# Optimization experiments

Hardware: AMD Instinct MI355X
Metric: run time of the kernel (lower is better)

## Reference

```python
import jax, jax.numpy as jnp
import numpy as np

T, D, L, H, N = 4096, 512, 10, 512, 40960  # tokens, feat dim, max span width, hidden, n_spans
LAMBDA = 0.4


def setup_inputs() -> dict:
    key = jax.random.key(0)
    ks = jax.random.split(key, 12)
    lin = lambda k, i, o: jax.random.normal(k, (i, o), jnp.float32) * 0.02
    return {
        "states": jax.random.normal(ks[0], (T, D), jnp.float32),
        "embeds": jax.random.normal(ks[1], (T, D), jnp.float32),
        "span_starts": jax.random.randint(ks[2], (N,), 0, T - L, jnp.int32),
        "span_widths": jax.random.randint(ks[3], (N,), 0, L, jnp.int32),
        "W_a1": lin(ks[4], D, H), "b_a1": jnp.zeros((H,), jnp.float32),
        "W_a2": lin(ks[5], H, H), "b_a2": jnp.zeros((H,), jnp.float32),
        "w_a3": lin(ks[6], H, 1), "b_a3": jnp.zeros((1,), jnp.float32),
        "W_s1": lin(ks[7], 3 * D, H), "b_s1": jnp.zeros((H,), jnp.float32),
        "W_s2": lin(ks[8], H, H), "b_s2": jnp.zeros((H,), jnp.float32),
        "w_s3": lin(ks[9], H, 1), "b_s3": jnp.zeros((1,), jnp.float32),
    }


def reference(states, embeds, span_starts, span_widths,
              W_a1, b_a1, W_a2, b_a2, w_a3, b_a3,
              W_s1, b_s1, W_s2, b_s2, w_s3, b_s3):
    # SpanAttention MLP: per-token attention logits [T]
    h = jax.nn.relu(states @ W_a1 + b_a1)
    h = jax.nn.relu(h @ W_a2 + b_a2)
    attns = (h @ w_a3 + b_a3)[:, 0]  # [T]

    # Ragged spans vectorized as fixed-width gather + mask.
    offs = jnp.arange(L, dtype=jnp.int32)            # [L]
    idx = span_starts[:, None] + offs[None, :]       # [N, L] token indices (in-range by construction)
    mask = offs[None, :] <= span_widths[:, None]     # [N, L]

    # Per-span masked softmax over attention logits (F.softmax(span_attn, dim=0)).
    logits = jnp.where(mask, attns[idx], -jnp.inf)
    w = jax.nn.softmax(logits, axis=1)               # [N, L]

    # Attention-weighted sum of word EMBEDDINGS over the span.
    attended = jnp.einsum('nl,nld->nd', w, embeds[idx])  # [N, D]

    ends = span_starts + span_widths                 # inclusive end index
    g = jnp.concatenate([states[span_starts], states[ends], attended], axis=-1)  # [N, 3D]

    # Mention score MLP
    s = jax.nn.relu(g @ W_s1 + b_s1)
    s = jax.nn.relu(s @ W_s2 + b_s2)
    scores = (s @ w_s3 + b_s3)[:, 0]                 # [N]

    # prune: keep top LAMBDA*T spans by score, sorted by index (Lee et al. 2017)
    k = int(LAMBDA * T)
    _, top_idx = jax.lax.top_k(scores, k)
    pruned_idx = jnp.sort(top_idx)
    return scores[pruned_idx], g, pruned_idx
```

## Files before the change

kernel.cpp:

```cpp
#include <hip/hip_runtime.h>
#include <hip/hip_bf16.h>
#include <stdint.h>

#define T_TOK 4096
#define D_DIM 512
#define L_SPAN 10
#define H_DIM 512
#define N_SPAN 40960
#define K_TOP 1638
#define CAND_CAP 6144
#define MARGIN 0.01f

typedef __attribute__((ext_vector_type(8))) short bf16x8;
typedef __attribute__((ext_vector_type(4))) float f32x4;

__device__ __forceinline__ ushort f2bf(float x) {
  uint32_t u = __float_as_uint(x);
  return (ushort)((u + 0x7FFFu + ((u >> 16) & 1u)) >> 16);
}
__device__ __forceinline__ float bf2f(ushort s) {
  return __uint_as_float(((uint32_t)s) << 16);
}

template <bool RELU, bool INDEXED>
__global__ __launch_bounds__(256) void sgemm32(
    const float* __restrict__ A, const float* __restrict__ B,
    const float* __restrict__ bias, float* __restrict__ C,
    int Kk, int lda, int ldb, int ldc,
    const uint32_t* __restrict__ rowCnt, const int* __restrict__ rowIdx) {
  const int BM = 32, BN = 64, BK = 32;
  __shared__ float As[BK][BM + 2];
  __shared__ float Bs[BK][BN + 4];

  int tid = threadIdx.x;
  int bn = blockIdx.x, bm = blockIdx.y;

  int cc = INDEXED ? 0 : 0x7fffffff;
  if (rowCnt) {
    cc = (int)*rowCnt;
    if (cc > CAND_CAP) cc = CAND_CAP;
    if (bm * BM >= ((cc + 31) & ~31)) return;
  }

  int tx = tid & 15, ty = tid >> 4;
  int a_m = tid >> 3;
  int a_k2 = tid & 7;
  int b_c4 = tid & 15;
  int b_kr = tid >> 4;

  int slot = bm * BM + a_m;
  const float* aRow;
  if (INDEXED) {
    int grow = (slot < cc) ? rowIdx[slot] : 0;
    aRow = A + (size_t)grow * lda;
  } else {
    aRow = A + (size_t)slot * lda;
  }
  const float* bPtr = B + (size_t)b_kr * ldb + bn * BN + b_c4 * 4;

  float acc[2][4];
#pragma unroll
  for (int i = 0; i < 2; ++i)
#pragma unroll
    for (int j = 0; j < 4; ++j) acc[i][j] = 0.f;

  for (int k0 = 0; k0 < Kk; k0 += BK) {
#pragma unroll
    for (int p = 0; p < 2; ++p) {
      float2 v = *(const float2*)(aRow + k0 + p * 16 + a_k2 * 2);
      As[p * 16 + a_k2 * 2 + 0][a_m] = v.x;
      As[p * 16 + a_k2 * 2 + 1][a_m] = v.y;
    }
#pragma unroll
    for (int p = 0; p < 2; ++p) {
      float4 v = *(const float4*)(bPtr + (size_t)(k0 + p * 16) * ldb);
      *(float4*)&Bs[b_kr + p * 16][b_c4 * 4] = v;
    }
    __syncthreads();

#pragma unroll
    for (int kk = 0; kk < BK; ++kk) {
      float2 a = *(const float2*)&As[kk][ty * 2];
      float4 b = *(const float4*)&Bs[kk][tx * 4];
      acc[0][0] = fmaf(a.x, b.x, acc[0][0]);
      acc[0][1] = fmaf(a.x, b.y, acc[0][1]);
      acc[0][2] = fmaf(a.x, b.z, acc[0][2]);
      acc[0][3] = fmaf(a.x, b.w, acc[0][3]);
      acc[1][0] = fmaf(a.y, b.x, acc[1][0]);
      acc[1][1] = fmaf(a.y, b.y, acc[1][1]);
      acc[1][2] = fmaf(a.y, b.z, acc[1][2]);
      acc[1][3] = fmaf(a.y, b.w, acc[1][3]);
    }
    __syncthreads();
  }

  int col0 = bn * BN + tx * 4;
  float4 bb = *(const float4*)(bias + col0);
#pragma unroll
  for (int i = 0; i < 2; ++i) {
    int row = bm * BM + ty * 2 + i;
    float o0 = acc[i][0] + bb.x;
    float o1 = acc[i][1] + bb.y;
    float o2 = acc[i][2] + bb.z;
    float o3 = acc[i][3] + bb.w;
    if (RELU) {
      o0 = fmaxf(o0, 0.f); o1 = fmaxf(o1, 0.f);
      o2 = fmaxf(o2, 0.f); o3 = fmaxf(o3, 0.f);
    }
    *(float4*)(C + (size_t)row * ldc + col0) = make_float4(o0, o1, o2, o3);
  }
}

__global__ __launch_bounds__(256) void mfma_gemm(
    const ushort* __restrict__ Ab, const ushort* __restrict__ Bb,
    const float* __restrict__ bias, ushort* __restrict__ Out,
    int K, int lda) {
  __shared__ ushort As[128][48];
  __shared__ ushort Bs[64][48];

  int wgl = blockIdx.x;
  int xcd = wgl & 7;
  int s = wgl >> 3;
  int p = ((s >> 3) << 3) | xcd;
  int bn = s & 7;
  int tid = threadIdx.x;
  int w = tid >> 6, l = tid & 63;
  int waveM = w & 1, waveN = w >> 1;
  int lr = l & 15, lg = l >> 4;
  int rowbase = p * 128;

  f32x4 acc[4][2];
#pragma unroll
  for (int m = 0; m < 4; ++m)
#pragma unroll
    for (int n = 0; n < 2; ++n)
#pragma unroll
      for (int r = 0; r < 4; ++r) acc[m][n][r] = 0.f;

  for (int k0 = 0; k0 < K; k0 += 32) {
#pragma unroll
    for (int it = 0; it < 2; ++it) {
      int idx = tid + it * 256;
      int ar = idx >> 2;
      int kc = (idx & 3) * 8;
      const ushort* src = Ab + (size_t)(rowbase + ar) * lda + k0 + kc;
      *(uint4*)&As[ar][kc] = *(const uint4*)src;
    }
    {
      int n = tid & 63;
      int kk0 = (tid >> 6) * 8;
#pragma unroll
      for (int i = 0; i < 8; ++i)
        Bs[n][kk0 + i] = Bb[(size_t)(k0 + kk0 + i) * 512 + bn * 64 + n];
    }
    __syncthreads();

    bf16x8 af[4], bv[2];
#pragma unroll
    for (int m = 0; m < 4; ++m)
      af[m] = *(const bf16x8*)&As[waveM * 64 + m * 16 + lr][lg * 8];
#pragma unroll
    for (int n = 0; n < 2; ++n)
      bv[n] = *(const bf16x8*)&Bs[waveN * 32 + n * 16 + lr][lg * 8];
#pragma unroll
    for (int m = 0; m < 4; ++m)
#pragma unroll
      for (int n = 0; n < 2; ++n)
        acc[m][n] = __builtin_amdgcn_mfma_f32_16x16x32_bf16(af[m], bv[n], acc[m][n], 0, 0, 0);
    __syncthreads();
  }

#pragma unroll
  for (int m = 0; m < 4; ++m) {
    int rg = rowbase + waveM * 64 + m * 16 + lg * 4;
#pragma unroll
    for (int n = 0; n < 2; ++n) {
      int cg = bn * 64 + waveN * 32 + n * 16 + lr;
      float bb = bias[cg];
#pragma unroll
      for (int r = 0; r < 4; ++r) {
        float v = fmaxf(acc[m][n][r] + bb, 0.f);
        Out[(size_t)(rg + r) * 512 + cg] = f2bf(v);
      }
    }
  }
}

__global__ void cvt_bf16_kernel(const float* __restrict__ src, ushort* __restrict__ dst, int n) {
  int i = blockIdx.x * blockDim.x + threadIdx.x;
  if (i < n) dst[i] = f2bf(src[i]);
}

__global__ __launch_bounds__(256) void rowdot_kernel(
    const float* __restrict__ X, const float* __restrict__ w,
    const float* __restrict__ b, float* __restrict__ out, int rows,
    const uint32_t* __restrict__ cnt) {
  int gid = blockIdx.x * blockDim.x + threadIdx.x;
  int wave = gid >> 6;
  int lane = threadIdx.x & 63;
  if (wave >= rows) return;
  if (cnt) {
    int cc = (int)*cnt;
    if (cc > CAND_CAP) cc = CAND_CAP;
    if (wave >= cc) return;
  }
  const float* x = X + (size_t)wave * H_DIM;
  float s = 0.f;
#pragma unroll
  for (int i = 0; i < 8; ++i) s = fmaf(x[lane + i * 64], w[lane + i * 64], s);
#pragma unroll
  for (int off = 32; off > 0; off >>= 1) s += __shfl_down(s, off);
  if (lane == 0) out[wave] = s + b[0];
}

__global__ __launch_bounds__(256) void rowdot_bf16_kernel(
    const ushort* __restrict__ X, const float* __restrict__ w,
    const float* __restrict__ b, float* __restrict__ out, int rows) {
  int gid = blockIdx.x * blockDim.x + threadIdx.x;
  int wave = gid >> 6;
  int lane = threadIdx.x & 63;
  if (wave >= rows) return;
  const ushort* x = X + (size_t)wave * H_DIM;
  float s = 0.f;
#pragma unroll
  for (int i = 0; i < 8; ++i) s = fmaf(bf2f(x[lane + i * 64]), w[lane + i * 64], s);
#pragma unroll
  for (int off = 32; off > 0; off >>= 1) s += __shfl_down(s, off);
  if (lane == 0) out[wave] = s + b[0];
}

__global__ __launch_bounds__(256) void span_kernel(
    const float* __restrict__ states, const float* __restrict__ embeds,
    const int* __restrict__ starts, const int* __restrict__ widths,
    const float* __restrict__ attns, float* __restrict__ g,
    ushort* __restrict__ g_bf) {
  int n = blockIdx.x;
  int tid = threadIdx.x;
  int st = starts[n];
  int wd = widths[n];

  float w[L_SPAN];
  float mx = -1e30f;
#pragma unroll
  for (int l = 0; l < L_SPAN; ++l) {
    float a = attns[st + l];
    a = (l <= wd) ? a : -1e30f;
    w[l] = a;
    mx = fmaxf(mx, a);
  }
  float ssum = 0.f;
#pragma unroll
  for (int l = 0; l < L_SPAN; ++l) {
    float e = expf(w[l] - mx);
    e = (l <= wd) ? e : 0.f;
    w[l] = e;
    ssum += e;
  }
  float inv = 1.f / ssum;

  int d = tid * 2;
  float2 att = make_float2(0.f, 0.f);
#pragma unroll
  for (int l = 0; l < L_SPAN; ++l) {
    float2 e = *(const float2*)(embeds + (size_t)(st + l) * D_DIM + d);
    float wl = w[l] * inv;
    att.x = fmaf(wl, e.x, att.x);
    att.y = fmaf(wl, e.y, att.y);
  }

  float* grow = g + (size_t)n * (3 * D_DIM);
  float2 s0 = *(const float2*)(states + (size_t)st * D_DIM + d);
  float2 s1 = *(const float2*)(states + (size_t)(st + wd) * D_DIM + d);
  *(float2*)(grow + d) = s0;
  *(float2*)(grow + D_DIM + d) = s1;
  *(float2*)(grow + 2 * D_DIM + d) = att;

  ushort* brow = g_bf + (size_t)n * (3 * D_DIM);
  ushort2 b0 = make_ushort2(f2bf(s0.x), f2bf(s0.y));
  ushort2 b1 = make_ushort2(f2bf(s1.x), f2bf(s1.y));
  ushort2 b2 = make_ushort2(f2bf(att.x), f2bf(att.y));
  *(ushort2*)(brow + d) = b0;
  *(ushort2*)(brow + D_DIM + d) = b1;
  *(ushort2*)(brow + 2 * D_DIM + d) = b2;
}

__global__ void keys_kernel(const float* __restrict__ scores, uint32_t* __restrict__ keys) {
  int n = blockIdx.x * blockDim.x + threadIdx.x;
  if (n < N_SPAN) {
    uint32_t u = __float_as_uint(scores[n]);
    keys[n] = (u & 0x80000000u) ? ~u : (u | 0x80000000u);
  }
}

__global__ void zero_kernel(uint32_t* __restrict__ p, int n) {
  int i = blockIdx.x * blockDim.x + threadIdx.x;
  if (i < n) p[i] = 0u;
}

__global__ void hist_hi_kernel(const uint32_t* __restrict__ keys, uint32_t* __restrict__ hist) {
  int n = blockIdx.x * blockDim.x + threadIdx.x;
  if (n < N_SPAN) atomicAdd(&hist[keys[n] >> 16], 1u);
}

__global__ void hist_lo_kernel(const uint32_t* __restrict__ keys,
                               const uint32_t* __restrict__ meta,
                               uint32_t* __restrict__ hist) {
  int n = blockIdx.x * blockDim.x + threadIdx.x;
  if (n < N_SPAN) {
    uint32_t k = keys[n];
    if ((k >> 16) == meta[0]) atomicAdd(&hist[k & 0xffffu], 1u);
  }
}

__global__ __launch_bounds__(1024) void select_kernel(
    const uint32_t* __restrict__ hist, uint32_t* __restrict__ meta, int level) {
  __shared__ uint32_t csum[1024];
  int tid = threadIdx.x;
  uint32_t Kwant = (level == 0) ? (uint32_t)K_TOP : meta[1];

  uint32_t s = 0;
  for (int j = 0; j < 64; ++j) s += hist[tid * 64 + j];
  csum[tid] = s;
  __syncthreads();
  for (int off = 1; off < 1024; off <<= 1) {
    uint32_t other = (tid + off < 1024) ? csum[tid + off] : 0u;
    __syncthreads();
    csum[tid] += other;
    __syncthreads();
  }
  if (csum[tid] >= Kwant && (tid == 1023 || csum[tid + 1] < Kwant)) {
    uint32_t running = (tid == 1023) ? 0u : csum[tid + 1];
    for (int j = 63; j >= 0; --j) {
      uint32_t h = hist[tid * 64 + j];
      if (running + h >= Kwant) {
        if (level == 0) {
          meta[0] = (uint32_t)(tid * 64 + j);
          meta[1] = Kwant - running;
        } else {
          meta[2] = (meta[0] << 16) | (uint32_t)(tid * 64 + j);
          meta[3] = Kwant - running;
        }
        break;
      }
      running += h;
    }
  }
}

__global__ void compact_cand(const uint32_t* __restrict__ keys, uint32_t* __restrict__ meta,
                             int* __restrict__ candIdx) {
  int n = blockIdx.x * blockDim.x + threadIdx.x;
  if (n >= N_SPAN) return;
  uint32_t tk = meta[2];
  uint32_t tu = (tk & 0x80000000u) ? (tk & 0x7FFFFFFFu) : ~tk;
  float tf = __uint_as_float(tu) - MARGIN;
  uint32_t mu = __float_as_uint(tf);
  uint32_t mk = (mu & 0x80000000u) ? ~mu : (mu | 0x80000000u);
  if (keys[n] >= mk) {
    uint32_t p = atomicAdd(&meta[6], 1u);
    if (p < CAND_CAP) candIdx[p] = n;
  }
}

__global__ __launch_bounds__(1024) void final_hybrid(
    const uint32_t* __restrict__ meta, const int* __restrict__ candIdx,
    const float* __restrict__ candExact,
    float* __restrict__ out_scores, float* __restrict__ out_idx) {
  __shared__ uint64_t pr[8192];
  int tid = threadIdx.x;
  int C = (int)meta[6];
  if (C > CAND_CAP) C = CAND_CAP;

  for (int i = tid; i < 8192; i += 1024) {
    uint64_t inv = ~0ULL;
    if (i < C) {
      uint32_t u = __float_as_uint(candExact[i]);
      uint32_t k = (u & 0x80000000u) ? ~u : (u | 0x80000000u);
      uint32_t orig = (uint32_t)candIdx[i];
      uint32_t low = ((0xFFFFu - orig) << 13) | (uint32_t)i;
      inv = ~(((uint64_t)k << 32) | low);
    }
    pr[i] = inv;
  }
  __syncthreads();
  for (int kk = 2; kk <= 8192; kk <<= 1) {
    for (int j = kk >> 1; j > 0; j >>= 1) {
      for (int t = tid; t < 8192; t += 1024) {
        int ixj = t ^ j;
        if (ixj > t) {
          bool up = ((t & kk) == 0);
          uint64_t a = pr[t], b = pr[ixj];
          if ((a > b) == up) { pr[t] = b; pr[ixj] = a; }
        }
      }
      __syncthreads();
    }
  }
  uint64_t mine[2];
#pragma unroll
  for (int t = 0; t < 2; ++t) {
    int i = tid + t * 1024;
    uint64_t v = ~pr[i];
    uint32_t low = (uint32_t)v;
    uint32_t orig = 0xFFFFu - ((low >> 13) & 0xFFFFu);
    uint32_t slot = low & 0x1FFFu;
    mine[t] = (i < K_TOP) ? (((uint64_t)orig << 32) | slot) : ~0ULL;
  }
  __syncthreads();
  pr[tid] = mine[0];
  pr[tid + 1024] = mine[1];
  __syncthreads();
  for (int kk = 2; kk <= 2048; kk <<= 1) {
    for (int j = kk >> 1; j > 0; j >>= 1) {
      for (int t = tid; t < 2048; t += 1024) {
        int ixj = t ^ j;
        if (ixj > t) {
          bool up = ((t & kk) == 0);
          uint64_t a = pr[t], b = pr[ixj];
          if ((a > b) == up) { pr[t] = b; pr[ixj] = a; }
        }
      }
      __syncthreads();
    }
  }
  for (int i = tid; i < K_TOP; i += 1024) {
    uint64_t v = pr[i];
    out_idx[i] = (float)(uint32_t)(v >> 32);
    out_scores[i] = candExact[v & 0x1FFFu];
  }
}

extern "C" void kernel_launch(void* const* d_in, const int* in_sizes, int n_in,
                              void* d_out, int out_size, void* d_ws, size_t ws_size,
                              hipStream_t stream) {
  const float* states = (const float*)d_in[0];
  const float* embeds = (const float*)d_in[1];
  const int* starts = (const int*)d_in[2];
  const int* widths = (const int*)d_in[3];
  const float* W_a1 = (const float*)d_in[4];
  const float* b_a1 = (const float*)d_in[5];
  const float* W_a2 = (const float*)d_in[6];
  const float* b_a2 = (const float*)d_in[7];
  const float* w_a3 = (const float*)d_in[8];
  const float* b_a3 = (const float*)d_in[9];
  const float* W_s1 = (const float*)d_in[10];
  const float* b_s1 = (const float*)d_in[11];
  const float* W_s2 = (const float*)d_in[12];
  const float* b_s2 = (const float*)d_in[13];
  const float* w_s3 = (const float*)d_in[14];
  const float* b_s3 = (const float*)d_in[15];

  float* out = (float*)d_out;
  float* out_scores = out;
  float* g = out + K_TOP;
  float* out_idx = out + K_TOP + (size_t)N_SPAN * 3 * D_DIM;

  char* ws = (char*)d_ws;
  const size_t MB = 1024 * 1024;
  ushort* g_bf = (ushort*)(ws + 0);
  ushort* s2b = (ushort*)(ws + 0);
  float* scoresA = (float*)(ws + 40 * MB);
  uint32_t* keys = (uint32_t*)(ws + 41 * MB);
  uint32_t* hist = (uint32_t*)(ws + 42 * MB);
  uint32_t* meta = hist + 65536;
  int* candIdx = (int*)(ws + 43 * MB);
  float* e1 = (float*)(ws + 80 * MB);
  float* e2 = (float*)(ws + 92 * MB);
  float* candExact = (float*)(ws + 104 * MB);
  float* h1 = (float*)(ws + 120 * MB);
  float* h2 = (float*)(ws + 128 * MB);
  float* attns = (float*)(ws + 136 * MB);
  ushort* s1b = (ushort*)(ws + 120 * MB);
  ushort* Wb1 = (ushort*)(ws + 160 * MB);
  ushort* Wb2 = (ushort*)(ws + 162 * MB);

  cvt_bf16_kernel<<<(3 * D_DIM * H_DIM) / 256, 256, 0, stream>>>(W_s1, Wb1, 3 * D_DIM * H_DIM);
  cvt_bf16_kernel<<<(H_DIM * H_DIM) / 256, 256, 0, stream>>>(W_s2, Wb2, H_DIM * H_DIM);

  sgemm32<true, false><<<dim3(H_DIM / 64, T_TOK / 32), 256, 0, stream>>>(
      states, W_a1, b_a1, h1, D_DIM, D_DIM, H_DIM, H_DIM, nullptr, nullptr);
  sgemm32<true, false><<<dim3(H_DIM / 64, T_TOK / 32), 256, 0, stream>>>(
      h1, W_a2, b_a2, h2, H_DIM, H_DIM, H_DIM, H_DIM, nullptr, nullptr);
  rowdot_kernel<<<T_TOK / 4, 256, 0, stream>>>(h2, w_a3, b_a3, attns, T_TOK, nullptr);

  span_kernel<<<N_SPAN, 256, 0, stream>>>(states, embeds, starts, widths, attns, g, g_bf);

  mfma_gemm<<<2560, 256, 0, stream>>>(g_bf, Wb1, b_s1, s1b, 3 * D_DIM, 3 * D_DIM);
  mfma_gemm<<<2560, 256, 0, stream>>>(s1b, Wb2, b_s2, s2b, H_DIM, H_DIM);
  rowdot_bf16_kernel<<<N_SPAN / 4, 256, 0, stream>>>(s2b, w_s3, b_s3, scoresA, N_SPAN);

  keys_kernel<<<N_SPAN / 256, 256, 0, stream>>>(scoresA, keys);
  zero_kernel<<<(65536 + 16 + 255) / 256, 256, 0, stream>>>(hist, 65536 + 16);
  hist_hi_kernel<<<N_SPAN / 256, 256, 0, stream>>>(keys, hist);
  select_kernel<<<1, 1024, 0, stream>>>(hist, meta, 0);
  zero_kernel<<<65536 / 256, 256, 0, stream>>>(hist, 65536);
  hist_lo_kernel<<<N_SPAN / 256, 256, 0, stream>>>(keys, meta, hist);
  select_kernel<<<1, 1024, 0, stream>>>(hist, meta, 1);

  compact_cand<<<N_SPAN / 256, 256, 0, stream>>>(keys, meta, candIdx);
  sgemm32<true, true><<<dim3(H_DIM / 64, CAND_CAP / 32), 256, 0, stream>>>(
      g, W_s1, b_s1, e1, 3 * D_DIM, 3 * D_DIM, H_DIM, H_DIM, meta + 6, candIdx);
  sgemm32<true, false><<<dim3(H_DIM / 64, CAND_CAP / 32), 256, 0, stream>>>(
      e1, W_s2, b_s2, e2, H_DIM, H_DIM, H_DIM, H_DIM, meta + 6, nullptr);
  rowdot_kernel<<<CAND_CAP / 4, 256, 0, stream>>>(e2, w_s3, b_s3, candExact, CAND_CAP, meta + 6);

  final_hybrid<<<1, 1024, 0, stream>>>(meta, candIdx, candExact, out_scores, out_idx);
}
```

Baseline: 991.5 us.

## Use 128x128 MFMA tiles with direct LDS loads and fuse score rowdot

Replaces the 128x64 bf16 MFMA GEMM with a 128x128 tile kernel that streams A and a pre-transposed weight matrix into LDS through global_load_lds, so the strided per-element B loads go away. The second GEMM now applies bias and ReLU and dots with w_s3 in its epilogue, reducing across lanes and adding into pre-initialised scores with atomics. This removes the s2 bf16 intermediate and the separate rowdot pass. The cost is a transpose-convert of the weights each call, float atomics whose summation order is nondeterministic, and a larger accumulator footprint.

```diff
diff --git a/kernel.cpp b/kernel.cpp
--- a/kernel.cpp
+++ b/kernel.cpp
@@ -20,6 +20,12 @@
 }
 __device__ __forceinline__ float bf2f(ushort s) {
   return __uint_as_float(((uint32_t)s) << 16);
+}
+
+__device__ __forceinline__ void gload16(const void* g, void* l) {
+  __builtin_amdgcn_global_load_lds(
+      (const __attribute__((address_space(1))) uint32_t*)g,
+      (__attribute__((address_space(3))) uint32_t*)l, 16, 0, 0);
 }
 
 template <bool RELU, bool INDEXED>
@@ -111,84 +117,121 @@
   }
 }
 
-__global__ __launch_bounds__(256) void mfma_gemm(
-    const ushort* __restrict__ Ab, const ushort* __restrict__ Bb,
-    const float* __restrict__ bias, ushort* __restrict__ Out,
-    int K, int lda) {
-  __shared__ ushort As[128][48];
-  __shared__ ushort Bs[64][48];
-
-  int wgl = blockIdx.x;
-  int xcd = wgl & 7;
-  int s = wgl >> 3;
-  int p = ((s >> 3) << 3) | xcd;
-  int bn = s & 7;
+template <bool FUSE>
+__global__ __launch_bounds__(256) void mfma128(
+    const ushort* __restrict__ Ab,
+    const ushort* __restrict__ BbT,
+    const float* __restrict__ bias,
+    ushort* __restrict__ Out,
+    const float* __restrict__ w3,
+    float* __restrict__ scoresA,
+    int K) {
+  __shared__ __align__(16) ushort As[4][128][8];
+  __shared__ __align__(16) ushort Bs[4][128][8];
+
+  int orig = blockIdx.x;
+  int xcd = orig & 7;
+  int s = orig >> 3;
+  int bn = s & 3;
+  int p = (s >> 2) * 8 + xcd;
+  int rowbase = p * 128;
+  int colbase = bn * 128;
+
   int tid = threadIdx.x;
   int w = tid >> 6, l = tid & 63;
   int waveM = w & 1, waveN = w >> 1;
   int lr = l & 15, lg = l >> 4;
-  int rowbase = p * 128;
-
-  f32x4 acc[4][2];
+
+  f32x4 acc[4][4];
 #pragma unroll
   for (int m = 0; m < 4; ++m)
 #pragma unroll
-    for (int n = 0; n < 2; ++n)
+    for (int n = 0; n < 4; ++n)
 #pragma unroll
       for (int r = 0; r < 4; ++r) acc[m][n][r] = 0.f;
 
+  const ushort* gA = Ab + (size_t)rowbase * K + w * 8;
+  const ushort* gB = BbT + (size_t)colbase * K + w * 8;
+
   for (int k0 = 0; k0 < K; k0 += 32) {
 #pragma unroll
-    for (int it = 0; it < 2; ++it) {
-      int idx = tid + it * 256;
-      int ar = idx >> 2;
-      int kc = (idx & 3) * 8;
-      const ushort* src = Ab + (size_t)(rowbase + ar) * lda + k0 + kc;
-      *(uint4*)&As[ar][kc] = *(const uint4*)src;
-    }
-    {
-      int n = tid & 63;
-      int kk0 = (tid >> 6) * 8;
-#pragma unroll
-      for (int i = 0; i < 8; ++i)
-        Bs[n][kk0 + i] = Bb[(size_t)(k0 + kk0 + i) * 512 + bn * 64 + n];
+    for (int i = 0; i < 2; ++i) {
+      int row = i * 64 + l;
+      gload16(gA + (size_t)row * K + k0, &As[w][i * 64][0]);
+      gload16(gB + (size_t)row * K + k0, &Bs[w][i * 64][0]);
     }
     __syncthreads();
 
-    bf16x8 af[4], bv[2];
+    bf16x8 af[4], bf[4];
 #pragma unroll
     for (int m = 0; m < 4; ++m)
-      af[m] = *(const bf16x8*)&As[waveM * 64 + m * 16 + lr][lg * 8];
-#pragma unroll
-    for (int n = 0; n < 2; ++n)
-      bv[n] = *(const bf16x8*)&Bs[waveN * 32 + n * 16 + lr][lg * 8];
+      af[m] = *(const bf16x8*)&As[lg][waveM * 64 + m * 16 + lr][0];
+#pragma unroll
+    for (int n = 0; n < 4; ++n)
+      bf[n] = *(const bf16x8*)&Bs[lg][waveN * 64 + n * 16 + lr][0];
 #pragma unroll
     for (int m = 0; m < 4; ++m)
 #pragma unroll
-      for (int n = 0; n < 2; ++n)
-        acc[m][n] = __builtin_amdgcn_mfma_f32_16x16x32_bf16(af[m], bv[n], acc[m][n], 0, 0, 0);
+      for (int n = 0; n < 4; ++n)
+        acc[m][n] = __builtin_amdgcn_mfma_f32_16x16x32_bf16(af[m], bf[n], acc[m][n], 0, 0, 0);
     __syncthreads();
   }
 
-#pragma unroll
-  for (int m = 0; m < 4; ++m) {
-    int rg = rowbase + waveM * 64 + m * 16 + lg * 4;
-#pragma unroll
-    for (int n = 0; n < 2; ++n) {
-      int cg = bn * 64 + waveN * 32 + n * 16 + lr;
-      float bb = bias[cg];
+  if (FUSE) {
+    float b2v[4], w3v[4];
+#pragma unroll
+    for (int n = 0; n < 4; ++n) {
+      int cg = colbase + waveN * 64 + n * 16 + lr;
+      b2v[n] = bias[cg];
+      w3v[n] = w3[cg];
+    }
+#pragma unroll
+    for (int m = 0; m < 4; ++m) {
 #pragma unroll
       for (int r = 0; r < 4; ++r) {
-        float v = fmaxf(acc[m][n][r] + bb, 0.f);
-        Out[(size_t)(rg + r) * 512 + cg] = f2bf(v);
+        float v = 0.f;
+#pragma unroll
+        for (int n = 0; n < 4; ++n)
+          v += fmaxf(acc[m][n][r] + b2v[n], 0.f) * w3v[n];
+        v += __shfl_xor(v, 1);
+        v += __shfl_xor(v, 2);
+        v += __shfl_xor(v, 4);
+        v += __shfl_xor(v, 8);
+        if (lr == 0)
+          atomicAdd(&scoresA[rowbase + waveM * 64 + m * 16 + lg * 4 + r], v);
       }
     }
-  }
-}
-
-__global__ void cvt_bf16_kernel(const float* __restrict__ src, ushort* __restrict__ dst, int n) {
+  } else {
+#pragma unroll
+    for (int m = 0; m < 4; ++m) {
+      int rg = rowbase + waveM * 64 + m * 16 + lg * 4;
+#pragma unroll
+      for (int n = 0; n < 4; ++n) {
+        int cg = colbase + waveN * 64 + n * 16 + lr;
+        float bb = bias[cg];
+#pragma unroll
+        for (int r = 0; r < 4; ++r) {
+          float v = fmaxf(acc[m][n][r] + bb, 0.f);
+          Out[(size_t)(rg + r) * 512 + cg] = f2bf(v);
+        }
+      }
+    }
+  }
+}
+
+__global__ void cvt_transpose_kernel(const float* __restrict__ W,
+                                     ushort* __restrict__ WT, int Kk, int Nn) {
   int i = blockIdx.x * blockDim.x + threadIdx.x;
-  if (i < n) dst[i] = f2bf(src[i]);
+  if (i < Kk * Nn) {
+    int k = i / Nn, n = i % Nn;
+    WT[(size_t)n * Kk + k] = f2bf(W[i]);
+  }
+}
+
+__global__ void init_scores_kernel(float* __restrict__ scoresA,
+                                   const float* __restrict__ b3) {
+  int i = blockIdx.x * blockDim.x + threadIdx.x;
+  if (i < N_SPAN) scoresA[i] = b3[0];
 }
 
 __global__ __launch_bounds__(256) void rowdot_kernel(
@@ -213,22 +256,6 @@
   if (lane == 0) out[wave] = s + b[0];
 }
 
-__global__ __launch_bounds__(256) void rowdot_bf16_kernel(
-    const ushort* __restrict__ X, const float* __restrict__ w,
-    const float* __restrict__ b, float* __restrict__ out, int rows) {
-  int gid = blockIdx.x * blockDim.x + threadIdx.x;
-  int wave = gid >> 6;
-  int lane = threadIdx.x & 63;
-  if (wave >= rows) return;
-  const ushort* x = X + (size_t)wave * H_DIM;
-  float s = 0.f;
-#pragma unroll
-  for (int i = 0; i < 8; ++i) s = fmaf(bf2f(x[lane + i * 64]), w[lane + i * 64], s);
-#pragma unroll
-  for (int off = 32; off > 0; off >>= 1) s += __shfl_down(s, off);
-  if (lane == 0) out[wave] = s + b[0];
-}
-
 __global__ __launch_bounds__(256) void span_kernel(
     const float* __restrict__ states, const float* __restrict__ embeds,
     const int* __restrict__ starts, const int* __restrict__ widths,
@@ -276,12 +303,9 @@
   *(float2*)(grow + 2 * D_DIM + d) = att;
 
   ushort* brow = g_bf + (size_t)n * (3 * D_DIM);
-  ushort2 b0 = make_ushort2(f2bf(s0.x), f2bf(s0.y));
-  ushort2 b1 = make_ushort2(f2bf(s1.x), f2bf(s1.y));
-  ushort2 b2 = make_ushort2(f2bf(att.x), f2bf(att.y));
-  *(ushort2*)(brow + d) = b0;
-  *(ushort2*)(brow + D_DIM + d) = b1;
-  *(ushort2*)(brow + 2 * D_DIM + d) = b2;
+  *(ushort2*)(brow + d) = make_ushort2(f2bf(s0.x), f2bf(s0.y));
+  *(ushort2*)(brow + D_DIM + d) = make_ushort2(f2bf(s1.x), f2bf(s1.y));
+  *(ushort2*)(brow + 2 * D_DIM + d) = make_ushort2(f2bf(att.x), f2bf(att.y));
 }
 
 __global__ void keys_kernel(const float* __restrict__ scores, uint32_t* __restrict__ keys) {
@@ -458,7 +482,6 @@
   char* ws = (char*)d_ws;
   const size_t MB = 1024 * 1024;
   ushort* g_bf = (ushort*)(ws + 0);
-  ushort* s2b = (ushort*)(ws + 0);
   float* scoresA = (float*)(ws + 40 * MB);
   uint32_t* keys = (uint32_t*)(ws + 41 * MB);
   uint32_t* hist = (uint32_t*)(ws + 42 * MB);
@@ -471,11 +494,13 @@
   float* h2 = (float*)(ws + 128 * MB);
   float* attns = (float*)(ws + 136 * MB);
   ushort* s1b = (ushort*)(ws + 120 * MB);
-  ushort* Wb1 = (ushort*)(ws + 160 * MB);
-  ushort* Wb2 = (ushort*)(ws + 162 * MB);
-
-  cvt_bf16_kernel<<<(3 * D_DIM * H_DIM) / 256, 256, 0, stream>>>(W_s1, Wb1, 3 * D_DIM * H_DIM);
-  cvt_bf16_kernel<<<(H_DIM * H_DIM) / 256, 256, 0, stream>>>(W_s2, Wb2, H_DIM * H_DIM);
+  ushort* W1T = (ushort*)(ws + 160 * MB);
+  ushort* W2T = (ushort*)(ws + 162 * MB);
+
+  cvt_transpose_kernel<<<(3 * D_DIM * H_DIM) / 256, 256, 0, stream>>>(
+      W_s1, W1T, 3 * D_DIM, H_DIM);
+  cvt_transpose_kernel<<<(H_DIM * H_DIM) / 256, 256, 0, stream>>>(
+      W_s2, W2T, H_DIM, H_DIM);
 
   sgemm32<true, false><<<dim3(H_DIM / 64, T_TOK / 32), 256, 0, stream>>>(
       states, W_a1, b_a1, h1, D_DIM, D_DIM, H_DIM, H_DIM, nullptr, nullptr);
@@ -485,9 +510,11 @@
 
   span_kernel<<<N_SPAN, 256, 0, stream>>>(states, embeds, starts, widths, attns, g, g_bf);
 
-  mfma_gemm<<<2560, 256, 0, stream>>>(g_bf, Wb1, b_s1, s1b, 3 * D_DIM, 3 * D_DIM);
-  mfma_gemm<<<2560, 256, 0, stream>>>(s1b, Wb2, b_s2, s2b, H_DIM, H_DIM);
-  rowdot_bf16_kernel<<<N_SPAN / 4, 256, 0, stream>>>(s2b, w_s3, b_s3, scoresA, N_SPAN);
+  mfma128<false><<<1280, 256, 0, stream>>>(
+      g_bf, W1T, b_s1, s1b, nullptr, nullptr, 3 * D_DIM);
+  init_scores_kernel<<<N_SPAN / 256, 256, 0, stream>>>(scoresA, b_s3);
+  mfma128<true><<<1280, 256, 0, stream>>>(
+      s1b, W2T, b_s2, nullptr, w_s3, scoresA, H_DIM);
 
   keys_kernel<<<N_SPAN / 256, 256, 0, stream>>>(scoresA, keys);
   zero_kernel<<<(65536 + 16 + 255) / 256, 256, 0, stream>>>(hist, 65536 + 16);
```

Measured after the change: 1.029 ms. 3.8% more time.
